# Optimization experiments

Hardware: AMD Instinct MI355X
Metric: run time of the kernel (lower is better)

Reference implementation:

```python
import jax, jax.numpy as jnp
import numpy as np

B = 64
L_IN = 4001
L_CONV = 998  # (4001-10)//4 + 1
D = 1000
EPS = 1e-5


def _convlin(x, cw, cb, lw, lb):
    # x: (B,1,4001), cw: (1,1,10), lw: (1000,998)
    y = jax.lax.conv_general_dilated(
        x, cw, window_strides=(4,), padding='VALID',
        dimension_numbers=('NCH', 'OIH', 'NCH')) + cb[None, :, None]  # (B,1,998)
    y = y @ lw.T + lb  # (B,1,1000)
    return jax.nn.relu(y)


def setup_inputs() -> dict:
    key = jax.random.key(0)
    ks = jax.random.split(key, 24)
    f32 = jnp.float32
    inp = {
        'x': jax.random.normal(ks[0], (B, 1, L_IN), dtype=f32),
        'bn_gamma': jnp.ones((L_IN,), f32),
        'bn_beta': jnp.zeros((L_IN,), f32),
        'bn_mean': jax.random.normal(ks[1], (L_IN,), f32) * 0.1,
        'bn_var': jax.random.uniform(ks[2], (L_IN,), f32, 0.5, 1.5),
        'conv_w_q': jax.random.normal(ks[3], (1, 1, 10), f32) * 0.3,
        'conv_b_q': jax.random.normal(ks[4], (1,), f32) * 0.1,
        'lin_w_q': jax.random.normal(ks[5], (D, L_CONV), f32) * (1.0 / np.sqrt(L_CONV)),
        'lin_b_q': jax.random.normal(ks[6], (D,), f32) * 0.02,
        'conv_w_k': jax.random.normal(ks[7], (1, 1, 10), f32) * 0.3,
        'conv_b_k': jax.random.normal(ks[8], (1,), f32) * 0.1,
        'lin_w_k': jax.random.normal(ks[9], (D, L_CONV), f32) * (1.0 / np.sqrt(L_CONV)),
        'lin_b_k': jax.random.normal(ks[10], (D,), f32) * 0.02,
        'conv_w_v': jax.random.normal(ks[11], (1, 1, 10), f32) * 0.3,
        'conv_b_v': jax.random.normal(ks[12], (1,), f32) * 0.1,
        'lin_w_v': jax.random.normal(ks[13], (D, L_CONV), f32) * (1.0 / np.sqrt(L_CONV)),
        'lin_b_v': jax.random.normal(ks[14], (D,), f32) * 0.02,
        'in_proj_w': jax.random.normal(ks[15], (3, 1), f32),
        'in_proj_b': jax.random.normal(ks[16], (3,), f32) * 0.02,
        'out_proj_w': jax.random.normal(ks[17], (1, 1), f32),
        'out_proj_b': jax.random.normal(ks[18], (1,), f32) * 0.02,
        'out_w': jax.random.normal(ks[19], (D, D), f32) * (1.0 / np.sqrt(D)),
        'out_b': jax.random.normal(ks[20], (D,), f32) * 0.02,
    }
    return inp


def reference(x, bn_gamma, bn_beta, bn_mean, bn_var,
              conv_w_q, conv_b_q, lin_w_q, lin_b_q,
              conv_w_k, conv_b_k, lin_w_k, lin_b_k,
              conv_w_v, conv_b_v, lin_w_v, lin_b_v,
              in_proj_w, in_proj_b, out_proj_w, out_proj_b,
              out_w, out_b):
    # BatchNorm1d over last dim (eval mode, running stats); x: (B,1,4001)
    xn = (x - bn_mean[None, None, :]) * jax.lax.rsqrt(bn_var[None, None, :] + EPS)
    xn = xn * bn_gamma[None, None, :] + bn_beta[None, None, :]

    Q = _convlin(xn, conv_w_q, conv_b_q, lin_w_q, lin_b_q)[:, 0, :]  # (B,1000)
    K = _convlin(xn, conv_w_k, conv_b_k, lin_w_k, lin_b_k)[:, 0, :]
    V = _convlin(xn, conv_w_v, conv_b_v, lin_w_v, lin_b_v)[:, 0, :]

    # MHA with embed_dim=1, num_heads=1 -> scalar in-projections, scale = 1
    q = Q * in_proj_w[0, 0] + in_proj_b[0]  # (B,1000)
    k = K * in_proj_w[1, 0] + in_proj_b[1]
    v = V * in_proj_w[2, 0] + in_proj_b[2]

    scores = q[:, :, None] * k[:, None, :]  # (B,1000,1000)
    attn = jax.nn.softmax(scores, axis=-1)
    ctx = jnp.einsum('bqk,bk->bq', attn, v)  # (B,1000)
    ctx = ctx * out_proj_w[0, 0] + out_proj_b[0]

    out = ctx[:, None, :] @ out_w.T + out_b  # (B,1,1000)
    return out
```

## Files before the change

### kernel.cpp

```cpp
#include <hip/hip_runtime.h>
#include <math.h>

#define NB 64
#define LIN 4001
#define LC 998
#define ND 1000
#define EPSBN 1e-5f

#define CK 96
#define NCH_LIN 11
#define NCH_OUT 11

#define OFF_CONVT 0u
#define OFF_PP    191616u
#define OFF_Q     2354304u
#define OFF_KV    2418304u
#define OFF_CF    2549376u
#define OFF_OP    2613376u

__global__ __launch_bounds__(256) void k_bnconv(
    const float* __restrict__ x,
    const float* __restrict__ g, const float* __restrict__ be,
    const float* __restrict__ mu, const float* __restrict__ va,
    const float* __restrict__ cwq, const float* __restrict__ cbq,
    const float* __restrict__ cwk, const float* __restrict__ cbk,
    const float* __restrict__ cwv, const float* __restrict__ cbv,
    float* __restrict__ convT)
{
    int j = blockIdx.x * 256 + threadIdx.x;
    int b = blockIdx.y;
    if (j >= LC) return;
    const float* xb = x + (size_t)b * LIN + 4 * j;
    float aq = 0.f, ak = 0.f, av = 0.f;
#pragma unroll
    for (int t = 0; t < 10; ++t) {
        int i = 4 * j + t;
        float s  = g[i] * rsqrtf(va[i] + EPSBN);
        float xn = (xb[t] - mu[i]) * s + be[i];
        aq = fmaf(xn, cwq[t], aq);
        ak = fmaf(xn, cwk[t], ak);
        av = fmaf(xn, cwv[t], av);
    }
    convT[((size_t)0 * LC + j) * 64 + b] = aq + cbq[0];
    convT[((size_t)1 * LC + j) * 64 + b] = ak + cbk[0];
    convT[((size_t)2 * LC + j) * 64 + b] = av + cbv[0];
}

__device__ __forceinline__ void gemm_tile(
    const float* __restrict__ Asrc,
    const float* __restrict__ Brow,
    int ldB, int dgb, int j0, int jc,
    float* __restrict__ Pt,
    float* lds)
{
    float* ldsC = lds;
    float* ldsW = lds + 6144;
    int tid  = threadIdx.x;
    int lane = tid & 63;
    int w    = tid >> 6;
    int b0   = (lane & 7) << 3;
    int d0   = (lane >> 3) << 3;

    {
        const float4* src = (const float4*)Asrc;
        float4* dst = (float4*)ldsC;
        for (int t = tid; t < jc * 16; t += 256) dst[t] = src[t];
    }
    for (int idx = tid; idx < 3072; idx += 256) {
        int dd = idx / 48, j2 = idx % 48;
        int dg = dgb + dd;
        float2 v = make_float2(0.f, 0.f);
        if (dg < ND && 2 * j2 < jc)
            v = *(const float2*)(Brow + (size_t)dg * ldB + j0 + 2 * j2);
        ldsW[dd * 97 + 2 * j2]     = v.x;
        ldsW[dd * 97 + 2 * j2 + 1] = v.y;
    }
    __syncthreads();

    float acc[8][8];
#pragma unroll
    for (int i = 0; i < 8; ++i)
#pragma unroll
        for (int jx = 0; jx < 8; ++jx) acc[i][jx] = 0.f;

    int js = (jc * w) >> 2;
    int je = (jc * (w + 1)) >> 2;
    for (int jj = js; jj < je; ++jj) {
        float4 c0 = *(const float4*)(ldsC + jj * 64 + b0);
        float4 c1 = *(const float4*)(ldsC + jj * 64 + b0 + 4);
        float cv[8] = {c0.x, c0.y, c0.z, c0.w, c1.x, c1.y, c1.z, c1.w};
        float wv[8];
#pragma unroll
        for (int r = 0; r < 8; ++r) wv[r] = ldsW[(d0 + r) * 97 + jj];
#pragma unroll
        for (int i = 0; i < 8; ++i)
#pragma unroll
            for (int jx = 0; jx < 8; ++jx)
                acc[i][jx] = fmaf(cv[i], wv[jx], acc[i][jx]);
    }
    __syncthreads();

    for (int p = 0; p < 2; ++p) {
        float* red = lds + w * 2304;
#pragma unroll
        for (int i = 0; i < 8; ++i)
            *(float4*)(red + (b0 + i) * 36 + (d0 >> 1)) =
                make_float4(acc[i][4*p], acc[i][4*p+1], acc[i][4*p+2], acc[i][4*p+3]);
        __syncthreads();
        for (int t = tid; t < 512; t += 256) {
            int bb = t >> 3, gg = t & 7;
            int o = bb * 36 + 4 * gg;
            float4 a0 = *(const float4*)(lds + o);
            float4 a1 = *(const float4*)(lds + 2304 + o);
            float4 a2 = *(const float4*)(lds + 4608 + o);
            float4 a3 = *(const float4*)(lds + 6912 + o);
            float4 s;
            s.x = a0.x + a1.x + a2.x + a3.x;
            s.y = a0.y + a1.y + a2.y + a3.y;
            s.z = a0.z + a1.z + a2.z + a3.z;
            s.w = a0.w + a1.w + a2.w + a3.w;
            *(float4*)(Pt + bb * 64 + 8 * gg + 4 * p) = s;
        }
        __syncthreads();
    }
}

__global__ __launch_bounds__(256) void k_lin(
    const float* __restrict__ convT,
    const float* __restrict__ lwq, const float* __restrict__ lwk,
    const float* __restrict__ lwv,
    float* __restrict__ Pp)
{
    __shared__ float lds[12352];
    int dgb   = blockIdx.x * 64;
    int which = blockIdx.y;
    int chunk = blockIdx.z;
    int j0 = chunk * CK;
    int jc = (LC - j0 < CK) ? (LC - j0) : CK;
    const float* lw = (which == 0) ? lwq : ((which == 1) ? lwk : lwv);
    const float* Asrc = convT + ((size_t)which * LC + j0) * 64;
    float* Pt = Pp + (((size_t)chunk * 3 + which) * 16 + blockIdx.x) * 4096;
    gemm_tile(Asrc, lw, LC, dgb, j0, jc, Pt, lds);
}

__global__ __launch_bounds__(256) void k_act(
    const float* __restrict__ Pp,
    const float* __restrict__ lbq, const float* __restrict__ lbk,
    const float* __restrict__ lbv,
    const float* __restrict__ ipw, const float* __restrict__ ipb,
    float* __restrict__ q, float* __restrict__ kv)
{
    int i = blockIdx.x * 256 + threadIdx.x;
    int b = blockIdx.y;
    if (i >= ND) return;
    int it = i >> 6, il = i & 63;
    float s0 = 0.f, s1 = 0.f, s2 = 0.f;
    for (int c = 0; c < NCH_LIN; ++c) {
        size_t base = (((size_t)c * 3) * 16 + it) * 4096 + (il | (b << 6));
        s0 += Pp[base];
        s1 += Pp[base + 16 * 4096];
        s2 += Pp[base + 32 * 4096];
    }
    float yq = fmaxf(s0 + lbq[i], 0.f) * ipw[0] + ipb[0];
    float yk = fmaxf(s1 + lbk[i], 0.f) * ipw[1] + ipb[1];
    float yv = fmaxf(s2 + lbv[i], 0.f) * ipw[2] + ipb[2];
    q[(size_t)b * ND + i] = yq;
    kv[(size_t)b * 2048 + 2 * i]     = yk;
    kv[(size_t)b * 2048 + 2 * i + 1] = yv;
}

__global__ __launch_bounds__(256) void k_attn(
    const float* __restrict__ q, const float* __restrict__ kv,
    const float* __restrict__ opw, const float* __restrict__ opb,
    float* __restrict__ cfT)
{
    __shared__ float ldsKV[2048];
    __shared__ float sden[256];
    __shared__ float snum[256];
    __shared__ float rmax[4];
    __shared__ float rmin[4];
    int tid = threadIdx.x;
    int b   = blockIdx.y;
    int w   = tid >> 6;
    int ii  = tid & 63;
    int i   = blockIdx.x * 64 + ii;

    {
        const float4* src = (const float4*)(kv + (size_t)b * 2048);
        float4* dst = (float4*)ldsKV;
        for (int t = tid; t < 512; t += 256) dst[t] = src[t];
    }
    __syncthreads();

    const float2* kv2 = (const float2*)ldsKV;
    float km = -INFINITY, kn = INFINITY;
    for (int idx = tid; idx < ND; idx += 256) {
        float2 f = kv2[idx];
        km = fmaxf(km, f.x);
        kn = fminf(kn, f.x);
    }
#pragma unroll
    for (int off = 1; off < 64; off <<= 1) {
        km = fmaxf(km, __shfl_xor(km, off));
        kn = fminf(kn, __shfl_xor(kn, off));
    }
    if (ii == 0) { rmax[w] = km; rmin[w] = kn; }
    __syncthreads();
    km = fmaxf(fmaxf(rmax[0], rmax[1]), fmaxf(rmax[2], rmax[3]));
    kn = fminf(fminf(rmin[0], rmin[1]), fminf(rmin[2], rmin[3]));

    float qi = (i < ND) ? q[(size_t)b * ND + i] : 0.f;
    float m  = (qi >= 0.f) ? qi * km : qi * kn;

    int jb = w * 250;
    float den = 0.f, num = 0.f;
#pragma unroll 2
    for (int jl = 0; jl < 250; ++jl) {
        float2 f = kv2[jb + jl];
        float e  = __expf(fmaf(qi, f.x, -m));
        den += e;
        num = fmaf(e, f.y, num);
    }
    sden[tid] = den;
    snum[tid] = num;
    __syncthreads();
    if (w == 0 && i < ND) {
        float dt = sden[ii] + sden[64 + ii] + sden[128 + ii] + sden[192 + ii];
        float nt = snum[ii] + snum[64 + ii] + snum[128 + ii] + snum[192 + ii];
        cfT[(size_t)i * 64 + b] = (nt / dt) * opw[0] + opb[0];
    }
}

__global__ __launch_bounds__(256) void k_out(
    const float* __restrict__ cfT, const float* __restrict__ W,
    float* __restrict__ Op)
{
    __shared__ float lds[12352];
    int egb   = blockIdx.x * 64;
    int chunk = blockIdx.y;
    int j0 = chunk * CK;
    int jc = (ND - j0 < CK) ? (ND - j0) : CK;
    const float* Asrc = cfT + (size_t)j0 * 64;
    float* Pt = Op + ((size_t)chunk * 16 + blockIdx.x) * 4096;
    gemm_tile(Asrc, W, ND, egb, j0, jc, Pt, lds);
}

__global__ __launch_bounds__(256) void k_fin(
    const float* __restrict__ Op, const float* __restrict__ outb,
    float* __restrict__ out)
{
    int e = blockIdx.x * 256 + threadIdx.x;
    int b = blockIdx.y;
    if (e >= ND) return;
    float s = outb[e];
    size_t cell = ((size_t)(e >> 6)) * 4096 + (b << 6) + (e & 63);
    for (int c = 0; c < NCH_OUT; ++c)
        s += Op[(size_t)c * 16 * 4096 + cell];
    out[(size_t)b * ND + e] = s;
}

extern "C" void kernel_launch(void* const* d_in, const int* in_sizes, int n_in,
                              void* d_out, int out_size, void* d_ws, size_t ws_size,
                              hipStream_t stream)
{
    const float* x    = (const float*)d_in[0];
    const float* g    = (const float*)d_in[1];
    const float* be   = (const float*)d_in[2];
    const float* mu   = (const float*)d_in[3];
    const float* va   = (const float*)d_in[4];
    const float* cwq  = (const float*)d_in[5];
    const float* cbq  = (const float*)d_in[6];
    const float* lwq  = (const float*)d_in[7];
    const float* lbq  = (const float*)d_in[8];
    const float* cwk  = (const float*)d_in[9];
    const float* cbk  = (const float*)d_in[10];
    const float* lwk  = (const float*)d_in[11];
    const float* lbk  = (const float*)d_in[12];
    const float* cwv  = (const float*)d_in[13];
    const float* cbv  = (const float*)d_in[14];
    const float* lwv  = (const float*)d_in[15];
    const float* lbv  = (const float*)d_in[16];
    const float* ipw  = (const float*)d_in[17];
    const float* ipb  = (const float*)d_in[18];
    const float* opw  = (const float*)d_in[19];
    const float* opb  = (const float*)d_in[20];
    const float* W    = (const float*)d_in[21];
    const float* outb = (const float*)d_in[22];

    float* ws    = (float*)d_ws;
    float* convT = ws + OFF_CONVT;
    float* Pp    = ws + OFF_PP;
    float* q     = ws + OFF_Q;
    float* kv    = ws + OFF_KV;
    float* cfT   = ws + OFF_CF;
    float* Op    = ws + OFF_OP;
    float* out   = (float*)d_out;

    k_bnconv<<<dim3(4, 64), 256, 0, stream>>>(x, g, be, mu, va,
                                              cwq, cbq, cwk, cbk, cwv, cbv, convT);
    k_lin  <<<dim3(16, 3, NCH_LIN), 256, 0, stream>>>(convT, lwq, lwk, lwv, Pp);
    k_act  <<<dim3(4, 64), 256, 0, stream>>>(Pp, lbq, lbk, lbv, ipw, ipb, q, kv);
    k_attn <<<dim3(16, 64), 256, 0, stream>>>(q, kv, opw, opb, cfT);
    k_out  <<<dim3(16, NCH_OUT), 256, 0, stream>>>(cfT, W, Op);
    k_fin  <<<dim3(4, 64), 256, 0, stream>>>(Op, outb, out);
}
```

Measured before the change: 170.0 us.

## Fuse all phases into one cooperative persistent kernel with grid syncs

```diff
diff --git a/kernel.cpp b/kernel.cpp
--- a/kernel.cpp
+++ b/kernel.cpp
@@ -1,5 +1,8 @@
 #include <hip/hip_runtime.h>
+#include <hip/hip_cooperative_groups.h>
 #include <math.h>
+
+namespace cg = cooperative_groups;
 
 #define NB 64
 #define LIN 4001
@@ -7,45 +10,29 @@
 #define ND 1000
 #define EPSBN 1e-5f
 
-#define CK 96
-#define NCH_LIN 11
-#define NCH_OUT 11
+#define CKL 100
+#define NCHL 10
+#define CKO 32
+#define NCHO 32
+#define GRID_BLOCKS 512
 
 #define OFF_CONVT 0u
 #define OFF_PP    191616u
-#define OFF_Q     2354304u
-#define OFF_KV    2418304u
-#define OFF_CF    2549376u
-#define OFF_OP    2613376u
-
-__global__ __launch_bounds__(256) void k_bnconv(
-    const float* __restrict__ x,
-    const float* __restrict__ g, const float* __restrict__ be,
-    const float* __restrict__ mu, const float* __restrict__ va,
-    const float* __restrict__ cwq, const float* __restrict__ cbq,
-    const float* __restrict__ cwk, const float* __restrict__ cbk,
-    const float* __restrict__ cwv, const float* __restrict__ cbv,
-    float* __restrict__ convT)
-{
-    int j = blockIdx.x * 256 + threadIdx.x;
-    int b = blockIdx.y;
-    if (j >= LC) return;
-    const float* xb = x + (size_t)b * LIN + 4 * j;
-    float aq = 0.f, ak = 0.f, av = 0.f;
-#pragma unroll
-    for (int t = 0; t < 10; ++t) {
-        int i = 4 * j + t;
-        float s  = g[i] * rsqrtf(va[i] + EPSBN);
-        float xn = (xb[t] - mu[i]) * s + be[i];
-        aq = fmaf(xn, cwq[t], aq);
-        ak = fmaf(xn, cwk[t], ak);
-        av = fmaf(xn, cwv[t], av);
-    }
-    convT[((size_t)0 * LC + j) * 64 + b] = aq + cbq[0];
-    convT[((size_t)1 * LC + j) * 64 + b] = ak + cbk[0];
-    convT[((size_t)2 * LC + j) * 64 + b] = av + cbv[0];
-}
-
+#define OFF_Q     2157696u
+#define OFF_KV    2221696u
+#define OFF_CF    2352768u
+#define OFF_OP    2416768u
+
+struct KParams {
+    const float *x, *g, *be, *mu, *va;
+    const float *cwq, *cbq, *lwq, *lbq;
+    const float *cwk, *cbk, *lwk, *lbk;
+    const float *cwv, *cbv, *lwv, *lbv;
+    const float *ipw, *ipb, *opw, *opb, *W, *outb;
+    float *convT, *Pp, *q, *kv, *cfT, *Op, *out;
+};
+
+template <int CKT>
 __device__ __forceinline__ void gemm_tile(
     const float* __restrict__ Asrc,
     const float* __restrict__ Brow,
@@ -53,8 +40,10 @@
     float* __restrict__ Pt,
     float* lds)
 {
+    constexpr int LDW = CKT + 1;
+    constexpr int F2R = CKT / 2;
     float* ldsC = lds;
-    float* ldsW = lds + 6144;
+    float* ldsW = lds + CKT * 64;
     int tid  = threadIdx.x;
     int lane = tid & 63;
     int w    = tid >> 6;
@@ -64,16 +53,17 @@
     {
         const float4* src = (const float4*)Asrc;
         float4* dst = (float4*)ldsC;
-        for (int t = tid; t < jc * 16; t += 256) dst[t] = src[t];
-    }
-    for (int idx = tid; idx < 3072; idx += 256) {
-        int dd = idx / 48, j2 = idx % 48;
+        int n = jc * 16;
+        for (int t = tid; t < n; t += 256) dst[t] = src[t];
+    }
+    for (int idx = tid; idx < 64 * F2R; idx += 256) {
+        int dd = idx / F2R, j2 = idx % F2R;
         int dg = dgb + dd;
         float2 v = make_float2(0.f, 0.f);
         if (dg < ND && 2 * j2 < jc)
             v = *(const float2*)(Brow + (size_t)dg * ldB + j0 + 2 * j2);
-        ldsW[dd * 97 + 2 * j2]     = v.x;
-        ldsW[dd * 97 + 2 * j2 + 1] = v.y;
+        ldsW[dd * LDW + 2 * j2]     = v.x;
+        ldsW[dd * LDW + 2 * j2 + 1] = v.y;
     }
     __syncthreads();
 
@@ -91,7 +81,7 @@
         float cv[8] = {c0.x, c0.y, c0.z, c0.w, c1.x, c1.y, c1.z, c1.w};
         float wv[8];
 #pragma unroll
-        for (int r = 0; r < 8; ++r) wv[r] = ldsW[(d0 + r) * 97 + jj];
+        for (int r = 0; r < 8; ++r) wv[r] = ldsW[(d0 + r) * LDW + jj];
 #pragma unroll
         for (int i = 0; i < 8; ++i)
 #pragma unroll
@@ -125,68 +115,73 @@
     }
 }
 
-__global__ __launch_bounds__(256) void k_lin(
-    const float* __restrict__ convT,
-    const float* __restrict__ lwq, const float* __restrict__ lwk,
-    const float* __restrict__ lwv,
-    float* __restrict__ Pp)
-{
-    __shared__ float lds[12352];
-    int dgb   = blockIdx.x * 64;
-    int which = blockIdx.y;
-    int chunk = blockIdx.z;
-    int j0 = chunk * CK;
-    int jc = (LC - j0 < CK) ? (LC - j0) : CK;
-    const float* lw = (which == 0) ? lwq : ((which == 1) ? lwk : lwv);
-    const float* Asrc = convT + ((size_t)which * LC + j0) * 64;
-    float* Pt = Pp + (((size_t)chunk * 3 + which) * 16 + blockIdx.x) * 4096;
-    gemm_tile(Asrc, lw, LC, dgb, j0, jc, Pt, lds);
-}
-
-__global__ __launch_bounds__(256) void k_act(
-    const float* __restrict__ Pp,
-    const float* __restrict__ lbq, const float* __restrict__ lbk,
-    const float* __restrict__ lbv,
-    const float* __restrict__ ipw, const float* __restrict__ ipb,
-    float* __restrict__ q, float* __restrict__ kv)
-{
-    int i = blockIdx.x * 256 + threadIdx.x;
-    int b = blockIdx.y;
-    if (i >= ND) return;
-    int it = i >> 6, il = i & 63;
-    float s0 = 0.f, s1 = 0.f, s2 = 0.f;
-    for (int c = 0; c < NCH_LIN; ++c) {
-        size_t base = (((size_t)c * 3) * 16 + it) * 4096 + (il | (b << 6));
-        s0 += Pp[base];
-        s1 += Pp[base + 16 * 4096];
-        s2 += Pp[base + 32 * 4096];
-    }
-    float yq = fmaxf(s0 + lbq[i], 0.f) * ipw[0] + ipb[0];
-    float yk = fmaxf(s1 + lbk[i], 0.f) * ipw[1] + ipb[1];
-    float yv = fmaxf(s2 + lbv[i], 0.f) * ipw[2] + ipb[2];
-    q[(size_t)b * ND + i] = yq;
-    kv[(size_t)b * 2048 + 2 * i]     = yk;
-    kv[(size_t)b * 2048 + 2 * i + 1] = yv;
-}
-
-__global__ __launch_bounds__(256) void k_attn(
-    const float* __restrict__ q, const float* __restrict__ kv,
-    const float* __restrict__ opw, const float* __restrict__ opb,
-    float* __restrict__ cfT)
-{
-    __shared__ float ldsKV[2048];
-    __shared__ float sden[256];
-    __shared__ float snum[256];
-    __shared__ float rmax[4];
-    __shared__ float rmin[4];
-    int tid = threadIdx.x;
-    int b   = blockIdx.y;
-    int w   = tid >> 6;
-    int ii  = tid & 63;
-    int i   = blockIdx.x * 64 + ii;
+__device__ __forceinline__ void ph_conv(const KParams& p, int jt, int b, int tid)
+{
+    int j = jt * 256 + tid;
+    if (j < LC) {
+        const float* xb = p.x + (size_t)b * LIN + 4 * j;
+        float aq = 0.f, ak = 0.f, av = 0.f;
+#pragma unroll
+        for (int t = 0; t < 10; ++t) {
+            int i = 4 * j + t;
+            float s  = p.g[i] * rsqrtf(p.va[i] + EPSBN);
+            float xn = (xb[t] - p.mu[i]) * s + p.be[i];
+            aq = fmaf(xn, p.cwq[t], aq);
+            ak = fmaf(xn, p.cwk[t], ak);
+            av = fmaf(xn, p.cwv[t], av);
+        }
+        p.convT[((size_t)0 * LC + j) * 64 + b] = aq + p.cbq[0];
+        p.convT[((size_t)1 * LC + j) * 64 + b] = ak + p.cbk[0];
+        p.convT[((size_t)2 * LC + j) * 64 + b] = av + p.cbv[0];
+    }
+}
+
+__device__ __forceinline__ void ph_lin(const KParams& p, int chunk, int which,
+                                       int dgx, float* smem)
+{
+    int j0 = chunk * CKL;
+    int jc = (LC - j0 < CKL) ? (LC - j0) : CKL;
+    const float* lw = (which == 0) ? p.lwq : ((which == 1) ? p.lwk : p.lwv);
+    const float* Asrc = p.convT + ((size_t)which * LC + j0) * 64;
+    float* Pt = p.Pp + (((size_t)chunk * 3 + which) * 16 + dgx) * 4096;
+    gemm_tile<CKL>(Asrc, lw, LC, dgx * 64, j0, jc, Pt, smem);
+}
+
+__device__ __forceinline__ void ph_act(const KParams& p, int it, int b, int tid)
+{
+    int i = it * 256 + tid;
+    if (i < ND) {
+        int ig = i >> 6, il = i & 63;
+        float s0 = 0.f, s1 = 0.f, s2 = 0.f;
+        for (int c = 0; c < NCHL; ++c) {
+            size_t base = (((size_t)c * 3) * 16 + ig) * 4096 + (il | (b << 6));
+            s0 += p.Pp[base];
+            s1 += p.Pp[base + 16 * 4096];
+            s2 += p.Pp[base + 32 * 4096];
+        }
+        float yq = fmaxf(s0 + p.lbq[i], 0.f) * p.ipw[0] + p.ipb[0];
+        float yk = fmaxf(s1 + p.lbk[i], 0.f) * p.ipw[1] + p.ipb[1];
+        float yv = fmaxf(s2 + p.lbv[i], 0.f) * p.ipw[2] + p.ipb[2];
+        p.q[(size_t)b * ND + i] = yq;
+        p.kv[(size_t)b * 2048 + 2 * i]     = yk;
+        p.kv[(size_t)b * 2048 + 2 * i + 1] = yv;
+    }
+}
+
+__device__ __forceinline__ void ph_attn(const KParams& p, int it, int b,
+                                        int tid, float* smem)
+{
+    float* ldsKV = smem;
+    float* sden  = smem + 2048;
+    float* snum  = smem + 2304;
+    float* rmax  = smem + 2560;
+    float* rmin  = smem + 2564;
+    int w  = tid >> 6;
+    int ii = tid & 63;
+    int i  = it * 64 + ii;
 
     {
-        const float4* src = (const float4*)(kv + (size_t)b * 2048);
+        const float4* src = (const float4*)(p.kv + (size_t)b * 2048);
         float4* dst = (float4*)ldsKV;
         for (int t = tid; t < 512; t += 256) dst[t] = src[t];
     }
@@ -209,7 +204,7 @@
     km = fmaxf(fmaxf(rmax[0], rmax[1]), fmaxf(rmax[2], rmax[3]));
     kn = fminf(fminf(rmin[0], rmin[1]), fminf(rmin[2], rmin[3]));
 
-    float qi = (i < ND) ? q[(size_t)b * ND + i] : 0.f;
+    float qi = (i < ND) ? p.q[(size_t)b * ND + i] : 0.f;
     float m  = (qi >= 0.f) ? qi * km : qi * kn;
 
     int jb = w * 250;
@@ -227,80 +222,137 @@
     if (w == 0 && i < ND) {
         float dt = sden[ii] + sden[64 + ii] + sden[128 + ii] + sden[192 + ii];
         float nt = snum[ii] + snum[64 + ii] + snum[128 + ii] + snum[192 + ii];
-        cfT[(size_t)i * 64 + b] = (nt / dt) * opw[0] + opb[0];
-    }
-}
-
-__global__ __launch_bounds__(256) void k_out(
-    const float* __restrict__ cfT, const float* __restrict__ W,
-    float* __restrict__ Op)
-{
-    __shared__ float lds[12352];
-    int egb   = blockIdx.x * 64;
-    int chunk = blockIdx.y;
-    int j0 = chunk * CK;
-    int jc = (ND - j0 < CK) ? (ND - j0) : CK;
-    const float* Asrc = cfT + (size_t)j0 * 64;
-    float* Pt = Op + ((size_t)chunk * 16 + blockIdx.x) * 4096;
-    gemm_tile(Asrc, W, ND, egb, j0, jc, Pt, lds);
-}
-
-__global__ __launch_bounds__(256) void k_fin(
-    const float* __restrict__ Op, const float* __restrict__ outb,
-    float* __restrict__ out)
-{
-    int e = blockIdx.x * 256 + threadIdx.x;
-    int b = blockIdx.y;
-    if (e >= ND) return;
-    float s = outb[e];
-    size_t cell = ((size_t)(e >> 6)) * 4096 + (b << 6) + (e & 63);
-    for (int c = 0; c < NCH_OUT; ++c)
-        s += Op[(size_t)c * 16 * 4096 + cell];
-    out[(size_t)b * ND + e] = s;
+        p.cfT[(size_t)i * 64 + b] = (nt / dt) * p.opw[0] + p.opb[0];
+    }
+    __syncthreads();
+}
+
+__device__ __forceinline__ void ph_out(const KParams& p, int chunk, int dgx,
+                                       float* smem)
+{
+    int j0 = chunk * CKO;
+    int jc = (ND - j0 < CKO) ? (ND - j0) : CKO;
+    const float* Asrc = p.cfT + (size_t)j0 * 64;
+    float* Pt = p.Op + ((size_t)chunk * 16 + dgx) * 4096;
+    gemm_tile<CKO>(Asrc, p.W, ND, dgx * 64, j0, jc, Pt, smem);
+}
+
+__device__ __forceinline__ void ph_fin(const KParams& p, int it, int b, int tid)
+{
+    int e = it * 256 + tid;
+    if (e < ND) {
+        float s = p.outb[e];
+        size_t cell = ((size_t)(e >> 6)) * 4096 + (b << 6) + (e & 63);
+        for (int c = 0; c < NCHO; ++c)
+            s += p.Op[(size_t)c * 16 * 4096 + cell];
+        p.out[(size_t)b * ND + e] = s;
+    }
+}
+
+__global__ __launch_bounds__(256, 3) void k_all(KParams p)
+{
+    __shared__ float smem[12864];
+    cg::grid_group grid = cg::this_grid();
+    const int tid = threadIdx.x;
+    const int bid = blockIdx.x;
+
+    if (bid < 256) ph_conv(p, bid & 3, bid >> 2, tid);
+    grid.sync();
+
+    if (bid < 480) {
+        int chunk = bid / 48, rem = bid % 48;
+        ph_lin(p, chunk, rem >> 4, rem & 15, smem);
+    }
+    grid.sync();
+
+    if (bid < 256) ph_act(p, bid & 3, bid >> 2, tid);
+    grid.sync();
+
+    for (int u = bid; u < 1024; u += GRID_BLOCKS)
+        ph_attn(p, u & 15, u >> 4, tid, smem);
+    grid.sync();
+
+    ph_out(p, bid >> 4, bid & 15, smem);
+    grid.sync();
+
+    if (bid < 256) ph_fin(p, bid & 3, bid >> 2, tid);
+}
+
+__global__ __launch_bounds__(256) void f_bnconv(KParams p)
+{
+    ph_conv(p, blockIdx.x, blockIdx.y, threadIdx.x);
+}
+__global__ __launch_bounds__(256) void f_lin(KParams p)
+{
+    __shared__ float smem[12864];
+    ph_lin(p, blockIdx.z, blockIdx.y, blockIdx.x, smem);
+}
+__global__ __launch_bounds__(256) void f_act(KParams p)
+{
+    ph_act(p, blockIdx.x, blockIdx.y, threadIdx.x);
+}
+__global__ __launch_bounds__(256) void f_attn(KParams p)
+{
+    __shared__ float smem[2568];
+    ph_attn(p, blockIdx.x, blockIdx.y, threadIdx.x, smem);
+}
+__global__ __launch_bounds__(256) void f_out(KParams p)
+{
+    __shared__ float smem[12864];
+    ph_out(p, blockIdx.y, blockIdx.x, smem);
+}
+__global__ __launch_bounds__(256) void f_fin(KParams p)
+{
+    ph_fin(p, blockIdx.x, blockIdx.y, threadIdx.x);
 }
 
 extern "C" void kernel_launch(void* const* d_in, const int* in_sizes, int n_in,
                               void* d_out, int out_size, void* d_ws, size_t ws_size,
                               hipStream_t stream)
 {
-    const float* x    = (const float*)d_in[0];
-    const float* g    = (const float*)d_in[1];
-    const float* be   = (const float*)d_in[2];
-    const float* mu   = (const float*)d_in[3];
-    const float* va   = (const float*)d_in[4];
-    const float* cwq  = (const float*)d_in[5];
-    const float* cbq  = (const float*)d_in[6];
-    const float* lwq  = (const float*)d_in[7];
-    const float* lbq  = (const float*)d_in[8];
-    const float* cwk  = (const float*)d_in[9];
-    const float* cbk  = (const float*)d_in[10];
-    const float* lwk  = (const float*)d_in[11];
-    const float* lbk  = (const float*)d_in[12];
-    const float* cwv  = (const float*)d_in[13];
-    const float* cbv  = (const float*)d_in[14];
-    const float* lwv  = (const float*)d_in[15];
-    const float* lbv  = (const float*)d_in[16];
-    const float* ipw  = (const float*)d_in[17];
-    const float* ipb  = (const float*)d_in[18];
-    const float* opw  = (const float*)d_in[19];
-    const float* opb  = (const float*)d_in[20];
-    const float* W    = (const float*)d_in[21];
-    const float* outb = (const float*)d_in[22];
-
-    float* ws    = (float*)d_ws;
-    float* convT = ws + OFF_CONVT;
-    float* Pp    = ws + OFF_PP;
-    float* q     = ws + OFF_Q;
-    float* kv    = ws + OFF_KV;
-    float* cfT   = ws + OFF_CF;
-    float* Op    = ws + OFF_OP;
-    float* out   = (float*)d_out;
-
-    k_bnconv<<<dim3(4, 64), 256, 0, stream>>>(x, g, be, mu, va,
-                                              cwq, cbq, cwk, cbk, cwv, cbv, convT);
-    k_lin  <<<dim3(16, 3, NCH_LIN), 256, 0, stream>>>(convT, lwq, lwk, lwv, Pp);
-    k_act  <<<dim3(4, 64), 256, 0, stream>>>(Pp, lbq, lbk, lbv, ipw, ipb, q, kv);
-    k_attn <<<dim3(16, 64), 256, 0, stream>>>(q, kv, opw, opb, cfT);
-    k_out  <<<dim3(16, NCH_OUT), 256, 0, stream>>>(cfT, W, Op);
-    k_fin  <<<dim3(4, 64), 256, 0, stream>>>(Op, outb, out);
-}
+    float* ws = (float*)d_ws;
+    KParams p;
+    p.x    = (const float*)d_in[0];
+    p.g    = (const float*)d_in[1];
+    p.be   = (const float*)d_in[2];
+    p.mu   = (const float*)d_in[3];
+    p.va   = (const float*)d_in[4];
+    p.cwq  = (const float*)d_in[5];
+    p.cbq  = (const float*)d_in[6];
+    p.lwq  = (const float*)d_in[7];
+    p.lbq  = (const float*)d_in[8];
+    p.cwk  = (const float*)d_in[9];
+    p.cbk  = (const float*)d_in[10];
+    p.lwk  = (const float*)d_in[11];
+    p.lbk  = (const float*)d_in[12];
+    p.cwv  = (const float*)d_in[13];
+    p.cbv  = (const float*)d_in[14];
+    p.lwv  = (const float*)d_in[15];
+    p.lbv  = (const float*)d_in[16];
+    p.ipw  = (const float*)d_in[17];
+    p.ipb  = (const float*)d_in[18];
+    p.opw  = (const float*)d_in[19];
+    p.opb  = (const float*)d_in[20];
+    p.W    = (const float*)d_in[21];
+    p.outb = (const float*)d_in[22];
+    p.convT = ws + OFF_CONVT;
+    p.Pp    = ws + OFF_PP;
+    p.q     = ws + OFF_Q;
+    p.kv    = ws + OFF_KV;
+    p.cfT   = ws + OFF_CF;
+    p.Op    = ws + OFF_OP;
+    p.out   = (float*)d_out;
+
+    void* args[] = { &p };
+    hipError_t e = hipLaunchCooperativeKernel((const void*)k_all,
+                                              dim3(GRID_BLOCKS), dim3(256),
+                                              args, 0, stream);
+    if (e != hipSuccess) {
+        f_bnconv<<<dim3(4, 64), 256, 0, stream>>>(p);
+        f_lin  <<<dim3(16, 3, NCHL), 256, 0, stream>>>(p);
+        f_act  <<<dim3(4, 64), 256, 0, stream>>>(p);
+        f_attn <<<dim3(16, 64), 256, 0, stream>>>(p);
+        f_out  <<<dim3(16, NCHO), 256, 0, stream>>>(p);
+        f_fin  <<<dim3(4, 64), 256, 0, stream>>>(p);
+    }
+}
```

Measured after the change: 477.4 us. +180.8%, slower.

## Fuse activation into attention kernel and retile linear GEMM chunks

Applied to the files above, without the earlier changes.

```diff
diff --git a/kernel.cpp b/kernel.cpp
--- a/kernel.cpp
+++ b/kernel.cpp
@@ -7,16 +7,15 @@
 #define ND 1000
 #define EPSBN 1e-5f
 
-#define CK 96
-#define NCH_LIN 11
-#define NCH_OUT 11
+#define CKL 100
+#define NCHL 10
+#define CKO 96
+#define NCHO 11
 
 #define OFF_CONVT 0u
 #define OFF_PP    191616u
-#define OFF_Q     2354304u
-#define OFF_KV    2418304u
-#define OFF_CF    2549376u
-#define OFF_OP    2613376u
+#define OFF_CF    2157696u
+#define OFF_OP    2221696u
 
 __global__ __launch_bounds__(256) void k_bnconv(
     const float* __restrict__ x,
@@ -46,6 +45,7 @@
     convT[((size_t)2 * LC + j) * 64 + b] = av + cbv[0];
 }
 
+template <int CKT>
 __device__ __forceinline__ void gemm_tile(
     const float* __restrict__ Asrc,
     const float* __restrict__ Brow,
@@ -53,8 +53,10 @@
     float* __restrict__ Pt,
     float* lds)
 {
+    constexpr int LDW = CKT + 1;
+    constexpr int F2R = CKT / 2;
     float* ldsC = lds;
-    float* ldsW = lds + 6144;
+    float* ldsW = lds + CKT * 64;
     int tid  = threadIdx.x;
     int lane = tid & 63;
     int w    = tid >> 6;
@@ -64,16 +66,17 @@
     {
         const float4* src = (const float4*)Asrc;
         float4* dst = (float4*)ldsC;
-        for (int t = tid; t < jc * 16; t += 256) dst[t] = src[t];
-    }
-    for (int idx = tid; idx < 3072; idx += 256) {
-        int dd = idx / 48, j2 = idx % 48;
+        int n = jc * 16;
+        for (int t = tid; t < n; t += 256) dst[t] = src[t];
+    }
+    for (int idx = tid; idx < 64 * F2R; idx += 256) {
+        int dd = idx / F2R, j2 = idx % F2R;
         int dg = dgb + dd;
         float2 v = make_float2(0.f, 0.f);
         if (dg < ND && 2 * j2 < jc)
             v = *(const float2*)(Brow + (size_t)dg * ldB + j0 + 2 * j2);
-        ldsW[dd * 97 + 2 * j2]     = v.x;
-        ldsW[dd * 97 + 2 * j2 + 1] = v.y;
+        ldsW[dd * LDW + 2 * j2]     = v.x;
+        ldsW[dd * LDW + 2 * j2 + 1] = v.y;
     }
     __syncthreads();
 
@@ -85,13 +88,14 @@
 
     int js = (jc * w) >> 2;
     int je = (jc * (w + 1)) >> 2;
+#pragma unroll 2
     for (int jj = js; jj < je; ++jj) {
         float4 c0 = *(const float4*)(ldsC + jj * 64 + b0);
         float4 c1 = *(const float4*)(ldsC + jj * 64 + b0 + 4);
         float cv[8] = {c0.x, c0.y, c0.z, c0.w, c1.x, c1.y, c1.z, c1.w};
         float wv[8];
 #pragma unroll
-        for (int r = 0; r < 8; ++r) wv[r] = ldsW[(d0 + r) * 97 + jj];
+        for (int r = 0; r < 8; ++r) wv[r] = ldsW[(d0 + r) * LDW + jj];
 #pragma unroll
         for (int i = 0; i < 8; ++i)
 #pragma unroll
@@ -131,64 +135,58 @@
     const float* __restrict__ lwv,
     float* __restrict__ Pp)
 {
-    __shared__ float lds[12352];
+    __shared__ float lds[12864];
     int dgb   = blockIdx.x * 64;
     int which = blockIdx.y;
     int chunk = blockIdx.z;
-    int j0 = chunk * CK;
-    int jc = (LC - j0 < CK) ? (LC - j0) : CK;
+    int j0 = chunk * CKL;
+    int jc = (LC - j0 < CKL) ? (LC - j0) : CKL;
     const float* lw = (which == 0) ? lwq : ((which == 1) ? lwk : lwv);
     const float* Asrc = convT + ((size_t)which * LC + j0) * 64;
     float* Pt = Pp + (((size_t)chunk * 3 + which) * 16 + blockIdx.x) * 4096;
-    gemm_tile(Asrc, lw, LC, dgb, j0, jc, Pt, lds);
-}
-
-__global__ __launch_bounds__(256) void k_act(
+    gemm_tile<CKL>(Asrc, lw, LC, dgb, j0, jc, Pt, lds);
+}
+
+__global__ __launch_bounds__(256) void k_actattn(
     const float* __restrict__ Pp,
     const float* __restrict__ lbq, const float* __restrict__ lbk,
     const float* __restrict__ lbv,
     const float* __restrict__ ipw, const float* __restrict__ ipb,
-    float* __restrict__ q, float* __restrict__ kv)
-{
-    int i = blockIdx.x * 256 + threadIdx.x;
-    int b = blockIdx.y;
-    if (i >= ND) return;
-    int it = i >> 6, il = i & 63;
-    float s0 = 0.f, s1 = 0.f, s2 = 0.f;
-    for (int c = 0; c < NCH_LIN; ++c) {
-        size_t base = (((size_t)c * 3) * 16 + it) * 4096 + (il | (b << 6));
-        s0 += Pp[base];
-        s1 += Pp[base + 16 * 4096];
-        s2 += Pp[base + 32 * 4096];
-    }
-    float yq = fmaxf(s0 + lbq[i], 0.f) * ipw[0] + ipb[0];
-    float yk = fmaxf(s1 + lbk[i], 0.f) * ipw[1] + ipb[1];
-    float yv = fmaxf(s2 + lbv[i], 0.f) * ipw[2] + ipb[2];
-    q[(size_t)b * ND + i] = yq;
-    kv[(size_t)b * 2048 + 2 * i]     = yk;
-    kv[(size_t)b * 2048 + 2 * i + 1] = yv;
-}
-
-__global__ __launch_bounds__(256) void k_attn(
-    const float* __restrict__ q, const float* __restrict__ kv,
     const float* __restrict__ opw, const float* __restrict__ opb,
     float* __restrict__ cfT)
 {
     __shared__ float ldsKV[2048];
-    __shared__ float sden[256];
-    __shared__ float snum[256];
     __shared__ float rmax[4];
     __shared__ float rmin[4];
     int tid = threadIdx.x;
+    int iq  = blockIdx.x;
     int b   = blockIdx.y;
     int w   = tid >> 6;
-    int ii  = tid & 63;
-    int i   = blockIdx.x * 64 + ii;
-
-    {
-        const float4* src = (const float4*)(kv + (size_t)b * 2048);
-        float4* dst = (float4*)ldsKV;
-        for (int t = tid; t < 512; t += 256) dst[t] = src[t];
+
+    for (int i = tid; i < ND; i += 256) {
+        int ig  = i >> 6;
+        int off = (i & 63) | (b << 6);
+        float s1 = 0.f, s2 = 0.f;
+#pragma unroll
+        for (int c = 0; c < NCHL; ++c) {
+            size_t base = (((size_t)c * 3 + 1) * 16 + ig) * 4096 + off;
+            s1 += Pp[base];
+            s2 += Pp[base + 16 * 4096];
+        }
+        ldsKV[2 * i]     = fmaxf(s1 + lbk[i], 0.f) * ipw[1] + ipb[1];
+        ldsKV[2 * i + 1] = fmaxf(s2 + lbv[i], 0.f) * ipw[2] + ipb[2];
+    }
+    int  i   = iq * 250 + tid;
+    bool act = (tid < 250);
+    float qi = 0.f;
+    if (act) {
+        int ig  = i >> 6;
+        int off = (i & 63) | (b << 6);
+        float s0 = 0.f;
+#pragma unroll
+        for (int c = 0; c < NCHL; ++c)
+            s0 += Pp[(((size_t)c * 3) * 16 + ig) * 4096 + off];
+        qi = fmaxf(s0 + lbq[i], 0.f) * ipw[0] + ipb[0];
     }
     __syncthreads();
 
@@ -204,31 +202,22 @@
         km = fmaxf(km, __shfl_xor(km, off));
         kn = fminf(kn, __shfl_xor(kn, off));
     }
-    if (ii == 0) { rmax[w] = km; rmin[w] = kn; }
+    if ((tid & 63) == 0) { rmax[w] = km; rmin[w] = kn; }
     __syncthreads();
     km = fmaxf(fmaxf(rmax[0], rmax[1]), fmaxf(rmax[2], rmax[3]));
     kn = fminf(fminf(rmin[0], rmin[1]), fminf(rmin[2], rmin[3]));
 
-    float qi = (i < ND) ? q[(size_t)b * ND + i] : 0.f;
-    float m  = (qi >= 0.f) ? qi * km : qi * kn;
-
-    int jb = w * 250;
+    float m = (qi >= 0.f) ? qi * km : qi * kn;
     float den = 0.f, num = 0.f;
-#pragma unroll 2
-    for (int jl = 0; jl < 250; ++jl) {
-        float2 f = kv2[jb + jl];
+#pragma unroll 4
+    for (int j = 0; j < ND; ++j) {
+        float2 f = kv2[j];
         float e  = __expf(fmaf(qi, f.x, -m));
         den += e;
         num = fmaf(e, f.y, num);
     }
-    sden[tid] = den;
-    snum[tid] = num;
-    __syncthreads();
-    if (w == 0 && i < ND) {
-        float dt = sden[ii] + sden[64 + ii] + sden[128 + ii] + sden[192 + ii];
-        float nt = snum[ii] + snum[64 + ii] + snum[128 + ii] + snum[192 + ii];
-        cfT[(size_t)i * 64 + b] = (nt / dt) * opw[0] + opb[0];
-    }
+    if (act)
+        cfT[(size_t)i * 64 + b] = (num / den) * opw[0] + opb[0];
 }
 
 __global__ __launch_bounds__(256) void k_out(
@@ -238,11 +227,11 @@
     __shared__ float lds[12352];
     int egb   = blockIdx.x * 64;
     int chunk = blockIdx.y;
-    int j0 = chunk * CK;
-    int jc = (ND - j0 < CK) ? (ND - j0) : CK;
+    int j0 = chunk * CKO;
+    int jc = (ND - j0 < CKO) ? (ND - j0) : CKO;
     const float* Asrc = cfT + (size_t)j0 * 64;
     float* Pt = Op + ((size_t)chunk * 16 + blockIdx.x) * 4096;
-    gemm_tile(Asrc, W, ND, egb, j0, jc, Pt, lds);
+    gemm_tile<CKO>(Asrc, W, ND, egb, j0, jc, Pt, lds);
 }
 
 __global__ __launch_bounds__(256) void k_fin(
@@ -254,7 +243,7 @@
     if (e >= ND) return;
     float s = outb[e];
     size_t cell = ((size_t)(e >> 6)) * 4096 + (b << 6) + (e & 63);
-    for (int c = 0; c < NCH_OUT; ++c)
+    for (int c = 0; c < NCHO; ++c)
         s += Op[(size_t)c * 16 * 4096 + cell];
     out[(size_t)b * ND + e] = s;
 }
@@ -290,17 +279,15 @@
     float* ws    = (float*)d_ws;
     float* convT = ws + OFF_CONVT;
     float* Pp    = ws + OFF_PP;
-    float* q     = ws + OFF_Q;
-    float* kv    = ws + OFF_KV;
     float* cfT   = ws + OFF_CF;
     float* Op    = ws + OFF_OP;
     float* out   = (float*)d_out;
 
-    k_bnconv<<<dim3(4, 64), 256, 0, stream>>>(x, g, be, mu, va,
-                                              cwq, cbq, cwk, cbk, cwv, cbv, convT);
-    k_lin  <<<dim3(16, 3, NCH_LIN), 256, 0, stream>>>(convT, lwq, lwk, lwv, Pp);
-    k_act  <<<dim3(4, 64), 256, 0, stream>>>(Pp, lbq, lbk, lbv, ipw, ipb, q, kv);
-    k_attn <<<dim3(16, 64), 256, 0, stream>>>(q, kv, opw, opb, cfT);
-    k_out  <<<dim3(16, NCH_OUT), 256, 0, stream>>>(cfT, W, Op);
-    k_fin  <<<dim3(4, 64), 256, 0, stream>>>(Op, outb, out);
-}
+    k_bnconv <<<dim3(4, 64), 256, 0, stream>>>(x, g, be, mu, va,
+                                               cwq, cbq, cwk, cbk, cwv, cbv, convT);
+    k_lin    <<<dim3(16, 3, NCHL), 256, 0, stream>>>(convT, lwq, lwk, lwv, Pp);
+    k_actattn<<<dim3(4, 64), 256, 0, stream>>>(Pp, lbq, lbk, lbv,
+                                               ipw, ipb, opw, opb, cfT);
+    k_out    <<<dim3(16, NCHO), 256, 0, stream>>>(cfT, W, Op);
+    k_fin    <<<dim3(4, 64), 256, 0, stream>>>(Op, outb, out);
+}
```

Result: slower. 178.1 us (+4.8%).
